# Kernel tuning notes

Hardware: AMD Instinct MI355X
Metric: run time of the kernel (lower is better)

The kernel has to match this reference:

```python
import jax, jax.numpy as jnp
import numpy as np

N_NODES = 32768
N_EDGES = 262144
HEAD = 8
CHANNEL = 64
LAYER_NUM = 2
HC = HEAD * CHANNEL  # 512


def setup_inputs() -> dict:
    key = jax.random.key(0)
    ks = jax.random.split(key, 12)
    def lin(k, fan_in, fan_out):
        s = 1.0 / np.sqrt(fan_in)
        kw, kb = jax.random.split(k)
        W = jax.random.uniform(kw, (fan_in, fan_out), jnp.float32, -s, s)
        b = jax.random.uniform(kb, (fan_out,), jnp.float32, -s, s)
        return W, b
    Wn, bn = lin(ks[0], 118, HC)
    We, be = lin(ks[1], 22, HC)
    Wa, ba = lin(ks[2], 2 * HC, HC)
    attn_w = jax.random.normal(ks[3], (1, HEAD, CHANNEL), jnp.float32) * 0.1
    x = jax.random.normal(ks[4], (N_NODES, 118), jnp.float32)
    edge_feat = jax.random.normal(ks[5], (N_EDGES, 22), jnp.float32)
    src = jax.random.randint(ks[6], (N_EDGES,), 0, N_NODES)
    dst = jax.random.randint(ks[7], (N_EDGES,), 0, N_NODES)
    return {"x": x, "edge_feat": edge_feat, "src": src, "dst": dst,
            "Wn": Wn, "bn": bn, "We": We, "be": be, "Wa": Wa, "ba": ba,
            "attn_w": attn_w}


def reference(x, edge_feat, src, dst, Wn, bn, We, be, Wa, ba, attn_w):
    N = x.shape[0]
    H, C = attn_w.shape[1], attn_w.shape[2]
    h = x @ Wn + bn                      # [N, H*C]
    _eh = edge_feat @ We + be            # computed in original forward, never used
    for _ in range(LAYER_NUM):
        # gather src/dst node states onto edges and score them (GATv2 style)
        e = jnp.concatenate([h[src], h[dst]], axis=-1)            # [E, 2HC]
        e = jax.nn.leaky_relu(e @ Wa + ba, negative_slope=0.01)   # [E, HC]
        score = jnp.sum(e.reshape(-1, H, C) * attn_w, axis=-1)    # [E, H]
        # edge softmax normalized over incoming edges of each dst node
        m = jax.ops.segment_max(score, dst, num_segments=N)       # [N, H]
        ex = jnp.exp(score - m[dst])                              # [E, H]
        denom = jax.ops.segment_sum(ex, dst, num_segments=N)      # [N, H]
        alpha = ex / denom[dst]                                   # [E, H]
        # weighted message passing: u_mul_e then sum over dst
        msg = h[src].reshape(-1, H, C) * alpha[:, :, None]        # [E, H, C]
        h = jax.ops.segment_sum(msg, dst, num_segments=N).reshape(N, H * C)
    return h
```

## Files before the change

kernel.cpp:

```cpp
#include <hip/hip_runtime.h>
#include <hip/hip_bf16.h>
#include <stdint.h>

#define N_NODES 32768
#define N_EDGES 262144

typedef __attribute__((ext_vector_type(8))) short short8;
typedef __attribute__((ext_vector_type(4))) float f32x4;
typedef __attribute__((ext_vector_type(4))) uint u32x4;

typedef const __attribute__((address_space(1))) void* gvp;
typedef __attribute__((address_space(3))) void* lvp;

#define LDH 1536
#define LDH2 1024

__device__ __forceinline__ float bf2f(ushort u) {
  return __uint_as_float(((uint)u) << 16);
}
__device__ __forceinline__ ushort f2bf(float f) {
  uint x = __float_as_uint(f);
  uint r = (x + 0x7fffu + ((x >> 16) & 1u)) >> 16;
  return (ushort)r;
}
__device__ __forceinline__ float loadf(const void* p, size_t i, int isbf) {
  return isbf ? bf2f(((const ushort*)p)[i]) : ((const float*)p)[i];
}

__global__ void detect_init(const uint* __restrict__ xw, int* __restrict__ flag,
                            int* __restrict__ cnt) {
  if (blockIdx.x > 0) {
    int i = (blockIdx.x - 1) * 256 + threadIdx.x;
    if (i < N_NODES) cnt[i] = 0;
    return;
  }
  __shared__ int c;
  if (threadIdx.x == 0) c = 0;
  __syncthreads();
  int good = 0;
  for (int i = threadIdx.x; i < 1024; i += 256) {
    uint lo = xw[i] & 0xFFFFu;
    uint ef = (lo >> 7) & 0xFFu;
    if (lo == 0u || (ef >= 0x60u && ef <= 0x90u)) good++;
  }
  atomicAdd(&c, good);
  __syncthreads();
  if (threadIdx.x == 0) *flag = (c >= 614) ? 1 : 0;
}

__global__ void prep_all(const void* __restrict__ Wa, const void* __restrict__ Wn,
                         const void* __restrict__ ba, const void* __restrict__ bn,
                         const void* __restrict__ aw, const void* __restrict__ x,
                         const int* __restrict__ flag, const int* __restrict__ dst,
                         ushort* __restrict__ W2T, ushort* __restrict__ BTc,
                         ushort* __restrict__ Wn_pad, float* __restrict__ bias2,
                         float* __restrict__ bnf, float* __restrict__ wf,
                         float* __restrict__ zbias, ushort* __restrict__ xp,
                         int* __restrict__ cnt) {
  const int b = blockIdx.x;
  if (b >= 2564 + 16384) {
    int e = (b - 2564 - 16384) * 256 + threadIdx.x;
    atomicAdd(&cnt[dst[e]], 1);
    return;
  }
  const int fl = *flag;
  if (b < 2048) {
    int t = b * 256 + threadIdx.x;
    int n = t >> 9, k = t & 511;
    size_t idx = (n < 512) ? ((size_t)k * 512 + n) : ((size_t)(512 + k) * 512 + (n - 512));
    W2T[t] = f2bf(loadf(Wa, idx, fl));
  } else if (b < 2304) {
    int t = (b - 2048) * 256 + threadIdx.x;
    int n = t >> 7, k = t & 127;
    BTc[t] = (k < 118) ? f2bf(loadf(Wn, (size_t)k * 512 + n, fl)) : (ushort)0;
  } else if (b < 2560) {
    int t = (b - 2304) * 256 + threadIdx.x;
    int n = t >> 9, j = t & 511;
    Wn_pad[t] = (n < 118) ? f2bf(loadf(Wn, (size_t)n * 512 + j, fl)) : (ushort)0;
  } else if (b < 2564) {
    int t = (b - 2560) * 256 + threadIdx.x;
    if (t < 1024) bias2[t] = (t < 512) ? loadf(ba, t, fl) : 0.f;
    if (t < 512) { bnf[t] = loadf(bn, t, fl); wf[t] = loadf(aw, t, fl); }
    if (t < 128) zbias[t] = 0.f;
  } else {
    int t = (b - 2564) * 256 + threadIdx.x;
    int i = t >> 7, k = t & 127;
    xp[t] = (k < 118) ? f2bf(loadf(x, (size_t)i * 118 + k, fl)) : (ushort)0;
  }
}

__device__ __forceinline__ void gemm_body(
    const ushort* __restrict__ A, const ushort* __restrict__ BT,
    const float* __restrict__ bias, ushort* __restrict__ C,
    int M, int N, int K, int lda, int ldc, int bx, int by) {
  __shared__ __align__(16) ushort As[128 * 32];
  __shared__ __align__(16) ushort Bs[128 * 32];
  const int tid = threadIdx.x, wave = tid >> 6, lane = tid & 63;
  const int bm = by * 128, bn = bx * 128;
  const int wm = (wave >> 1) * 64, wn = (wave & 1) * 64;
  const int fcol = lane & 15, quad = lane >> 4;

  const f32x4 zero = {0.f, 0.f, 0.f, 0.f};
  f32x4 acc[4][4];
#pragma unroll
  for (int i = 0; i < 4; ++i)
#pragma unroll
    for (int j = 0; j < 4; ++j) acc[i][j] = zero;

  for (int k0 = 0; k0 < K; k0 += 32) {
#pragma unroll
    for (int r = 0; r < 2; ++r) {
      int o = r * 4096 + wave * 1024 + lane * 16;
      int row = o >> 6;
      int ke = (o & 63) >> 1;
      const ushort* gA = A + (size_t)(bm + row) * lda + k0 + ke;
      const ushort* gB = BT + (size_t)(bn + row) * K + k0 + ke;
      ushort* lA = As + ((r * 4096 + wave * 1024) >> 1);
      ushort* lB = Bs + ((r * 4096 + wave * 1024) >> 1);
      __builtin_amdgcn_global_load_lds((gvp)(const void*)gA, (lvp)(void*)lA, 16, 0, 0);
      __builtin_amdgcn_global_load_lds((gvp)(const void*)gB, (lvp)(void*)lB, 16, 0, 0);
    }
    __syncthreads();
    short8 a[4], b[4];
#pragma unroll
    for (int i = 0; i < 4; ++i) {
      a[i] = *(const short8*)&As[(wm + i * 16 + fcol) * 32 + quad * 8];
      b[i] = *(const short8*)&Bs[(wn + i * 16 + fcol) * 32 + quad * 8];
    }
#pragma unroll
    for (int i = 0; i < 4; ++i)
#pragma unroll
      for (int j = 0; j < 4; ++j)
        acc[i][j] = __builtin_amdgcn_mfma_f32_16x16x32_bf16(a[i], b[j], acc[i][j], 0, 0, 0);
    __syncthreads();
  }

#pragma unroll
  for (int i = 0; i < 4; ++i) {
    int rowb = bm + wm + i * 16 + quad * 4;
#pragma unroll
    for (int j = 0; j < 4; ++j) {
      int col = bn + wn + j * 16 + fcol;
      float bb = bias[col];
#pragma unroll
      for (int r = 0; r < 4; ++r) {
        C[(size_t)(rowb + r) * ldc + col] = f2bf(acc[i][j][r] + bb);
      }
    }
  }
}

__global__ __launch_bounds__(256)
void mid_kernel(const ushort* __restrict__ W2T, const ushort* __restrict__ Wn_pad,
                const float* __restrict__ bnf, const float* __restrict__ bias2,
                const float* __restrict__ zbias, float* __restrict__ bcomb,
                ushort* __restrict__ BTc, const int* __restrict__ cnt,
                int* __restrict__ rowptr, int* __restrict__ cursor) {
  const int b = blockIdx.x;
  if (b < 256) {
    const int tid = b * 256 + threadIdx.x;
    if (tid < 512) bcomb[tid] = bnf[tid];
    const int wave = threadIdx.x >> 6, lane = threadIdx.x & 63;
    const int j = b * 4 + wave;
    const uint4 v = *(const uint4*)(W2T + (size_t)j * 512 + lane * 8);
    const float4 b0 = *(const float4*)(bnf + lane * 8);
    const float4 b1 = *(const float4*)(bnf + lane * 8 + 4);
    const uint w[4] = {v.x, v.y, v.z, v.w};
    const float bb[8] = {b0.x, b0.y, b0.z, b0.w, b1.x, b1.y, b1.z, b1.w};
    float s = 0.f;
#pragma unroll
    for (int i = 0; i < 4; ++i) {
      s += __uint_as_float(w[i] << 16) * bb[2 * i];
      s += __uint_as_float(w[i] & 0xffff0000u) * bb[2 * i + 1];
    }
    s += __shfl_xor(s, 1);  s += __shfl_xor(s, 2);  s += __shfl_xor(s, 4);
    s += __shfl_xor(s, 8);  s += __shfl_xor(s, 16); s += __shfl_xor(s, 32);
    if (lane == 0) bcomb[512 + j] = s + bias2[j];
  } else if (b < 264) {
    gemm_body(W2T, Wn_pad, zbias, BTc + 512 * 128, 1024, 128, 512, 512, 128,
              0, b - 256);
  } else {
    __shared__ int part[256];
    const int t = threadIdx.x;
    const int base = t * 128;
    int s = 0;
    for (int i = 0; i < 128; ++i) s += cnt[base + i];
    part[t] = s;
    __syncthreads();
    for (int off = 1; off < 256; off <<= 1) {
      int v = (t >= off) ? part[t - off] : 0;
      __syncthreads();
      part[t] += v;
      __syncthreads();
    }
    int run = (t == 0) ? 0 : part[t - 1];
    for (int i = 0; i < 128; ++i) {
      int v = cnt[base + i];
      rowptr[base + i] = run;
      cursor[base + i] = run;
      run += v;
    }
    if (t == 255) rowptr[N_NODES] = part[255];
  }
}

__global__ __launch_bounds__(256)
void fill_gemm(const int* __restrict__ dst, const int* __restrict__ src,
               int* __restrict__ cursor, int* __restrict__ esrc,
               const ushort* __restrict__ xp, const ushort* __restrict__ BTc,
               const float* __restrict__ bcomb, ushort* __restrict__ HP) {
  const int b = blockIdx.x;
  if (b < 1024) {
    int e = b * 256 + threadIdx.x;
    int p = atomicAdd(&cursor[dst[e]], 1);
    esrc[p] = src[e];
    return;
  }
  const int gi = b - 1024;
  gemm_body(xp, BTc, bcomb, HP, N_NODES, 1536, 128, 128, LDH, gi % 12, gi / 12);
}

__global__ __launch_bounds__(256)
void node_fused_l1(const ushort* __restrict__ HP, const int* __restrict__ esrc,
                   const int* __restrict__ rowptr, const float* __restrict__ wf,
                   const float* __restrict__ bias2, ushort* __restrict__ HP2,
                   ushort* __restrict__ Q2arr) {
  const int wave = threadIdx.x >> 6, lane = threadIdx.x & 63;
  const int d = blockIdx.x * 4 + wave;
  const int beg = rowptr[d], end = rowptr[d + 1];
  const int c0 = lane * 8;

  const uint4 qv = *(const uint4*)(HP + (size_t)d * LDH + 1024 + c0);
  const uint qw[4] = {qv.x, qv.y, qv.z, qv.w};
  float q[8], w[8];
#pragma unroll
  for (int i = 0; i < 4; ++i) {
    q[2 * i]     = __uint_as_float(qw[i] << 16);
    q[2 * i + 1] = __uint_as_float(qw[i] & 0xffff0000u);
  }
  const float4 w0 = *(const float4*)(wf + c0);
  const float4 w1 = *(const float4*)(wf + c0 + 4);
  w[0] = w0.x; w[1] = w0.y; w[2] = w0.z; w[3] = w0.w;
  w[4] = w1.x; w[5] = w1.y; w[6] = w1.z; w[7] = w1.w;

  float m = -3e38f, den = 0.f;
  float aP[8], aQ[8], aH[8];
#pragma unroll
  for (int i = 0; i < 8; ++i) { aP[i] = 0.f; aQ[i] = 0.f; aH[i] = 0.f; }

  if (beg < end) {
    int sj = esrc[beg];
    for (int j = beg; j < end; ++j) {
      const int s = sj;
      if (j + 1 < end) sj = esrc[j + 1];
      const ushort* row = HP + (size_t)s * LDH;
      const uint4 hv = *(const uint4*)(row + c0);
      const uint4 pa = *(const uint4*)(row + 512 + c0);
      const uint4 pb = *(const uint4*)(row + 1024 + c0);
      const uint paw[4] = {pa.x, pa.y, pa.z, pa.w};
      const uint pbw[4] = {pb.x, pb.y, pb.z, pb.w};
      const uint hw[4]  = {hv.x, hv.y, hv.z, hv.w};
      float t = 0.f;
#pragma unroll
      for (int i = 0; i < 4; ++i) {
        float ea = __uint_as_float(paw[i] << 16) + q[2 * i];
        float eb = __uint_as_float(paw[i] & 0xffff0000u) + q[2 * i + 1];
        ea = (ea > 0.f) ? ea : 0.01f * ea;
        eb = (eb > 0.f) ? eb : 0.01f * eb;
        t += ea * w[2 * i] + eb * w[2 * i + 1];
      }
      t += __shfl_xor(t, 1);
      t += __shfl_xor(t, 2);
      t += __shfl_xor(t, 4);
      if (__any(t > m)) {
        const float mnew = fmaxf(m, t);
        const float corr = __expf(m - mnew);
        const float ex = __expf(t - mnew);
        den = den * corr + ex;
#pragma unroll
        for (int i = 0; i < 4; ++i) {
          aP[2 * i]     = aP[2 * i] * corr     + ex * __uint_as_float(paw[i] << 16);
          aP[2 * i + 1] = aP[2 * i + 1] * corr + ex * __uint_as_float(paw[i] & 0xffff0000u);
          aQ[2 * i]     = aQ[2 * i] * corr     + ex * __uint_as_float(pbw[i] << 16);
          aQ[2 * i + 1] = aQ[2 * i + 1] * corr + ex * __uint_as_float(pbw[i] & 0xffff0000u);
          aH[2 * i]     = aH[2 * i] * corr     + ex * __uint_as_float(hw[i] << 16);
          aH[2 * i + 1] = aH[2 * i + 1] * corr + ex * __uint_as_float(hw[i] & 0xffff0000u);
        }
        m = mnew;
      } else {
        const float ex = __expf(t - m);
        den += ex;
#pragma unroll
        for (int i = 0; i < 4; ++i) {
          aP[2 * i]     += ex * __uint_as_float(paw[i] << 16);
          aP[2 * i + 1] += ex * __uint_as_float(paw[i] & 0xffff0000u);
          aQ[2 * i]     += ex * __uint_as_float(pbw[i] << 16);
          aQ[2 * i + 1] += ex * __uint_as_float(pbw[i] & 0xffff0000u);
          aH[2 * i]     += ex * __uint_as_float(hw[i] << 16);
          aH[2 * i + 1] += ex * __uint_as_float(hw[i] & 0xffff0000u);
        }
      }
    }
  }

  const int deg = end - beg;
  const float inv = deg ? (1.f / den) : 0.f;
  const float4 bp0 = *(const float4*)(bias2 + c0);
  const float4 bp1 = *(const float4*)(bias2 + c0 + 4);
  const float bp[8] = {bp0.x, bp0.y, bp0.z, bp0.w, bp1.x, bp1.y, bp1.z, bp1.w};
  uint oP[4], oQ[4], oH[4];
#pragma unroll
  for (int i = 0; i < 4; ++i) {
    float p0 = deg ? aP[2 * i] * inv : bp[2 * i];
    float p1 = deg ? aP[2 * i + 1] * inv : bp[2 * i + 1];
    float q0 = deg ? aQ[2 * i] * inv : 0.f;
    float q1 = deg ? aQ[2 * i + 1] * inv : 0.f;
    float h0v = aH[2 * i] * inv, h1v = aH[2 * i + 1] * inv;
    oP[i] = (uint)f2bf(p0) | ((uint)f2bf(p1) << 16);
    oQ[i] = (uint)f2bf(q0) | ((uint)f2bf(q1) << 16);
    oH[i] = (uint)f2bf(h0v) | ((uint)f2bf(h1v) << 16);
  }
  u32x4 vP = {oP[0], oP[1], oP[2], oP[3]};
  u32x4 vQ = {oQ[0], oQ[1], oQ[2], oQ[3]};
  u32x4 vH = {oH[0], oH[1], oH[2], oH[3]};
  ushort* orow = HP2 + (size_t)d * LDH2;
  *(u32x4*)(orow + c0) = vH;
  *(u32x4*)(orow + 512 + c0) = vP;
  *(u32x4*)(Q2arr + (size_t)d * 512 + c0) = vQ;
}

__global__ __launch_bounds__(256)
void node_fused_l2(const ushort* __restrict__ HP2, const ushort* __restrict__ Q2arr,
                   const int* __restrict__ esrc, const int* __restrict__ rowptr,
                   const float* __restrict__ wf, const int* __restrict__ flag,
                   void* __restrict__ out) {
  const int wave = threadIdx.x >> 6, lane = threadIdx.x & 63;
  const int d = blockIdx.x * 4 + wave;
  const int beg = rowptr[d], end = rowptr[d + 1];
  const int c0 = lane * 8;

  const uint4 qv = *(const uint4*)(Q2arr + (size_t)d * 512 + c0);
  const uint qw[4] = {qv.x, qv.y, qv.z, qv.w};
  float q[8], w[8];
#pragma unroll
  for (int i = 0; i < 4; ++i) {
    q[2 * i]     = __uint_as_float(qw[i] << 16);
    q[2 * i + 1] = __uint_as_float(qw[i] & 0xffff0000u);
  }
  const float4 w0 = *(const float4*)(wf + c0);
  const float4 w1 = *(const float4*)(wf + c0 + 4);
  w[0] = w0.x; w[1] = w0.y; w[2] = w0.z; w[3] = w0.w;
  w[4] = w1.x; w[5] = w1.y; w[6] = w1.z; w[7] = w1.w;

  float m = -3e38f, den = 0.f;
  float acc[8] = {0.f, 0.f, 0.f, 0.f, 0.f, 0.f, 0.f, 0.f};

  if (beg < end) {
    int sj = esrc[beg];
    for (int j = beg; j < end; ++j) {
      const int s = sj;
      if (j + 1 < end) sj = esrc[j + 1];
      const ushort* row = HP2 + (size_t)s * LDH2;
      const uint4 hv = *(const uint4*)(row + c0);
      const uint4 pv = *(const uint4*)(row + 512 + c0);
      const uint pw[4] = {pv.x, pv.y, pv.z, pv.w};
      const uint hw[4] = {hv.x, hv.y, hv.z, hv.w};
      float t = 0.f;
#pragma unroll
      for (int i = 0; i < 4; ++i) {
        float ea = __uint_as_float(pw[i] << 16) + q[2 * i];
        float eb = __uint_as_float(pw[i] & 0xffff0000u) + q[2 * i + 1];
        ea = (ea > 0.f) ? ea : 0.01f * ea;
        eb = (eb > 0.f) ? eb : 0.01f * eb;
        t += ea * w[2 * i] + eb * w[2 * i + 1];
      }
      t += __shfl_xor(t, 1);
      t += __shfl_xor(t, 2);
      t += __shfl_xor(t, 4);
      if (__any(t > m)) {
        const float mnew = fmaxf(m, t);
        const float corr = __expf(m - mnew);
        const float ex = __expf(t - mnew);
        den = den * corr + ex;
#pragma unroll
        for (int i = 0; i < 4; ++i) {
          acc[2 * i]     = acc[2 * i] * corr     + ex * __uint_as_float(hw[i] << 16);
          acc[2 * i + 1] = acc[2 * i + 1] * corr + ex * __uint_as_float(hw[i] & 0xffff0000u);
        }
        m = mnew;
      } else {
        const float ex = __expf(t - m);
        den += ex;
#pragma unroll
        for (int i = 0; i < 4; ++i) {
          acc[2 * i]     += ex * __uint_as_float(hw[i] << 16);
          acc[2 * i + 1] += ex * __uint_as_float(hw[i] & 0xffff0000u);
        }
      }
    }
  }

  const float inv = (end > beg) ? (1.f / den) : 0.f;
  if (*flag) {
    uint o[4];
#pragma unroll
    for (int i = 0; i < 4; ++i) {
      float v0 = acc[2 * i] * inv, v1 = acc[2 * i + 1] * inv;
      o[i] = (uint)f2bf(v0) | ((uint)f2bf(v1) << 16);
    }
    u32x4 ov = {o[0], o[1], o[2], o[3]};
    __builtin_nontemporal_store(ov, (u32x4*)((ushort*)out + (size_t)d * 512 + c0));
  } else {
    f32x4 f0 = {acc[0] * inv, acc[1] * inv, acc[2] * inv, acc[3] * inv};
    f32x4 f1 = {acc[4] * inv, acc[5] * inv, acc[6] * inv, acc[7] * inv};
    __builtin_nontemporal_store(f0, (f32x4*)((float*)out + (size_t)d * 512 + c0));
    __builtin_nontemporal_store(f1, (f32x4*)((float*)out + (size_t)d * 512 + c0 + 4));
  }
}

extern "C" void kernel_launch(void* const* d_in, const int* in_sizes, int n_in,
                              void* d_out, int out_size, void* d_ws, size_t ws_size,
                              hipStream_t stream) {
  const void* x   = d_in[0];
  const int*  src = (const int*)d_in[2];
  const int*  dst = (const int*)d_in[3];
  const void* Wn  = d_in[4];
  const void* bn  = d_in[5];
  const void* Wa  = d_in[8];
  const void* ba  = d_in[9];
  const void* aw  = d_in[10];

  char* ws = (char*)d_ws;
  size_t off = 0;
  auto alloc = [&](size_t bytes) {
    char* p = ws + off;
    off = (off + bytes + 255) & ~(size_t)255;
    return p;
  };
  ushort* HP     = (ushort*)alloc((size_t)N_NODES * LDH * 2);
  ushort* HP2    = (ushort*)alloc((size_t)N_NODES * LDH2 * 2);
  ushort* Q2arr  = (ushort*)alloc((size_t)N_NODES * 512 * 2);
  int*    esrc   = (int*)   alloc((size_t)N_EDGES * 4);
  int*    rowptr = (int*)   alloc((size_t)(N_NODES + 1) * 4);
  int*    cnt    = (int*)   alloc((size_t)N_NODES * 4);
  int*    cursor = (int*)   alloc((size_t)N_NODES * 4);
  ushort* W2T    = (ushort*)alloc((size_t)1024 * 512 * 2);
  ushort* BTc    = (ushort*)alloc((size_t)1536 * 128 * 2);
  ushort* Wn_pad = (ushort*)alloc((size_t)128 * 512 * 2);
  float*  bias2  = (float*) alloc(1024 * 4);
  float*  bcomb  = (float*) alloc(1536 * 4);
  float*  zbias  = (float*) alloc(128 * 4);
  ushort* xp     = (ushort*)alloc((size_t)N_NODES * 128 * 2);
  float*  bnf    = (float*) alloc(512 * 4);
  float*  wf     = (float*) alloc(512 * 4);
  int*    flag   = (int*)   alloc(256);

  detect_init<<<1 + 128, 256, 0, stream>>>((const uint*)x, flag, cnt);
  prep_all<<<2564 + 16384 + 1024, 256, 0, stream>>>(
      Wa, Wn, ba, bn, aw, x, flag, dst, W2T, BTc, Wn_pad, bias2, bnf, wf, zbias,
      xp, cnt);
  mid_kernel<<<256 + 8 + 1, 256, 0, stream>>>(W2T, Wn_pad, bnf, bias2, zbias,
                                              bcomb, BTc, cnt, rowptr, cursor);
  fill_gemm<<<1024 + 12 * 256, 256, 0, stream>>>(dst, src, cursor, esrc, xp, BTc,
                                                 bcomb, HP);
  node_fused_l1<<<N_NODES / 4, 256, 0, stream>>>(HP, esrc, rowptr, wf, bias2,
                                                 HP2, Q2arr);
  node_fused_l2<<<N_NODES / 4, 256, 0, stream>>>(HP2, Q2arr, esrc, rowptr, wf,
                                                 flag, d_out);
}
```

Measured before the change: 406.5 us.

## Compute layer-2 Q projection with a node GEMM instead of per-edge aggregation

The layer-1 kernel stops gathering and aggregating the precomputed Q-projection slice for every edge. The layer-2 query term is now computed after aggregation by a separate dense GEMM over the aggregated node features. The first GEMM's Q columns go to a separate array so gathered rows shrink from 1536 to 1024 elements. This cuts per-edge gather bandwidth and FMAs, at the cost of an extra kernel launch and a 32768x512x512 GEMM. It also relies on bias2+512 being zero, which holds for how bias2 is initialized.

```diff
diff --git a/kernel.cpp b/kernel.cpp
--- a/kernel.cpp
+++ b/kernel.cpp
@@ -12,7 +12,7 @@
 typedef const __attribute__((address_space(1))) void* gvp;
 typedef __attribute__((address_space(3))) void* lvp;
 
-#define LDH 1536
+#define LDH1 1024
 #define LDH2 1024
 
 __device__ __forceinline__ float bf2f(ushort u) {
@@ -92,7 +92,7 @@
 __device__ __forceinline__ void gemm_body(
     const ushort* __restrict__ A, const ushort* __restrict__ BT,
     const float* __restrict__ bias, ushort* __restrict__ C,
-    int M, int N, int K, int lda, int ldc, int bx, int by) {
+    int K, int lda, int ldc, int bx, int by, int col_off) {
   __shared__ __align__(16) ushort As[128 * 32];
   __shared__ __align__(16) ushort Bs[128 * 32];
   const int tid = threadIdx.x, wave = tid >> 6, lane = tid & 63;
@@ -144,7 +144,7 @@
       float bb = bias[col];
 #pragma unroll
       for (int r = 0; r < 4; ++r) {
-        C[(size_t)(rowb + r) * ldc + col] = f2bf(acc[i][j][r] + bb);
+        C[(size_t)(rowb + r) * ldc + (col - col_off)] = f2bf(acc[i][j][r] + bb);
       }
     }
   }
@@ -177,8 +177,7 @@
     s += __shfl_xor(s, 8);  s += __shfl_xor(s, 16); s += __shfl_xor(s, 32);
     if (lane == 0) bcomb[512 + j] = s + bias2[j];
   } else if (b < 264) {
-    gemm_body(W2T, Wn_pad, zbias, BTc + 512 * 128, 1024, 128, 512, 512, 128,
-              0, b - 256);
+    gemm_body(W2T, Wn_pad, zbias, BTc + 512 * 128, 512, 512, 128, 0, b - 256, 0);
   } else {
     __shared__ int part[256];
     const int t = threadIdx.x;
@@ -208,7 +207,8 @@
 void fill_gemm(const int* __restrict__ dst, const int* __restrict__ src,
                int* __restrict__ cursor, int* __restrict__ esrc,
                const ushort* __restrict__ xp, const ushort* __restrict__ BTc,
-               const float* __restrict__ bcomb, ushort* __restrict__ HP) {
+               const float* __restrict__ bcomb, ushort* __restrict__ HPa,
+               ushort* __restrict__ Q1arr) {
   const int b = blockIdx.x;
   if (b < 1024) {
     int e = b * 256 + threadIdx.x;
@@ -217,20 +217,24 @@
     return;
   }
   const int gi = b - 1024;
-  gemm_body(xp, BTc, bcomb, HP, N_NODES, 1536, 128, 128, LDH, gi % 12, gi / 12);
+  const int bx = gi % 12, by = gi / 12;
+  if (bx < 8)
+    gemm_body(xp, BTc, bcomb, HPa, 128, 128, LDH1, bx, by, 0);
+  else
+    gemm_body(xp, BTc, bcomb, Q1arr, 128, 128, 512, bx, by, 1024);
 }
 
 __global__ __launch_bounds__(256)
-void node_fused_l1(const ushort* __restrict__ HP, const int* __restrict__ esrc,
-                   const int* __restrict__ rowptr, const float* __restrict__ wf,
-                   const float* __restrict__ bias2, ushort* __restrict__ HP2,
-                   ushort* __restrict__ Q2arr) {
+void node_fused_l1(const ushort* __restrict__ HPa, const ushort* __restrict__ Q1arr,
+                   const int* __restrict__ esrc, const int* __restrict__ rowptr,
+                   const float* __restrict__ wf, const float* __restrict__ bias2,
+                   ushort* __restrict__ HP2) {
   const int wave = threadIdx.x >> 6, lane = threadIdx.x & 63;
   const int d = blockIdx.x * 4 + wave;
   const int beg = rowptr[d], end = rowptr[d + 1];
   const int c0 = lane * 8;
 
-  const uint4 qv = *(const uint4*)(HP + (size_t)d * LDH + 1024 + c0);
+  const uint4 qv = *(const uint4*)(Q1arr + (size_t)d * 512 + c0);
   const uint qw[4] = {qv.x, qv.y, qv.z, qv.w};
   float q[8], w[8];
 #pragma unroll
@@ -244,21 +248,19 @@
   w[4] = w1.x; w[5] = w1.y; w[6] = w1.z; w[7] = w1.w;
 
   float m = -3e38f, den = 0.f;
-  float aP[8], aQ[8], aH[8];
-#pragma unroll
-  for (int i = 0; i < 8; ++i) { aP[i] = 0.f; aQ[i] = 0.f; aH[i] = 0.f; }
+  float aP[8], aH[8];
+#pragma unroll
+  for (int i = 0; i < 8; ++i) { aP[i] = 0.f; aH[i] = 0.f; }
 
   if (beg < end) {
     int sj = esrc[beg];
     for (int j = beg; j < end; ++j) {
       const int s = sj;
       if (j + 1 < end) sj = esrc[j + 1];
-      const ushort* row = HP + (size_t)s * LDH;
+      const ushort* row = HPa + (size_t)s * LDH1;
       const uint4 hv = *(const uint4*)(row + c0);
       const uint4 pa = *(const uint4*)(row + 512 + c0);
-      const uint4 pb = *(const uint4*)(row + 1024 + c0);
       const uint paw[4] = {pa.x, pa.y, pa.z, pa.w};
-      const uint pbw[4] = {pb.x, pb.y, pb.z, pb.w};
       const uint hw[4]  = {hv.x, hv.y, hv.z, hv.w};
       float t = 0.f;
 #pragma unroll
@@ -281,8 +283,6 @@
         for (int i = 0; i < 4; ++i) {
           aP[2 * i]     = aP[2 * i] * corr     + ex * __uint_as_float(paw[i] << 16);
           aP[2 * i + 1] = aP[2 * i + 1] * corr + ex * __uint_as_float(paw[i] & 0xffff0000u);
-          aQ[2 * i]     = aQ[2 * i] * corr     + ex * __uint_as_float(pbw[i] << 16);
-          aQ[2 * i + 1] = aQ[2 * i + 1] * corr + ex * __uint_as_float(pbw[i] & 0xffff0000u);
           aH[2 * i]     = aH[2 * i] * corr     + ex * __uint_as_float(hw[i] << 16);
           aH[2 * i + 1] = aH[2 * i + 1] * corr + ex * __uint_as_float(hw[i] & 0xffff0000u);
         }
@@ -294,8 +294,6 @@
         for (int i = 0; i < 4; ++i) {
           aP[2 * i]     += ex * __uint_as_float(paw[i] << 16);
           aP[2 * i + 1] += ex * __uint_as_float(paw[i] & 0xffff0000u);
-          aQ[2 * i]     += ex * __uint_as_float(pbw[i] << 16);
-          aQ[2 * i + 1] += ex * __uint_as_float(pbw[i] & 0xffff0000u);
           aH[2 * i]     += ex * __uint_as_float(hw[i] << 16);
           aH[2 * i + 1] += ex * __uint_as_float(hw[i] & 0xffff0000u);
         }
@@ -308,25 +306,27 @@
   const float4 bp0 = *(const float4*)(bias2 + c0);
   const float4 bp1 = *(const float4*)(bias2 + c0 + 4);
   const float bp[8] = {bp0.x, bp0.y, bp0.z, bp0.w, bp1.x, bp1.y, bp1.z, bp1.w};
-  uint oP[4], oQ[4], oH[4];
+  uint oP[4], oH[4];
 #pragma unroll
   for (int i = 0; i < 4; ++i) {
     float p0 = deg ? aP[2 * i] * inv : bp[2 * i];
     float p1 = deg ? aP[2 * i + 1] * inv : bp[2 * i + 1];
-    float q0 = deg ? aQ[2 * i] * inv : 0.f;
-    float q1 = deg ? aQ[2 * i + 1] * inv : 0.f;
     float h0v = aH[2 * i] * inv, h1v = aH[2 * i + 1] * inv;
     oP[i] = (uint)f2bf(p0) | ((uint)f2bf(p1) << 16);
-    oQ[i] = (uint)f2bf(q0) | ((uint)f2bf(q1) << 16);
     oH[i] = (uint)f2bf(h0v) | ((uint)f2bf(h1v) << 16);
   }
   u32x4 vP = {oP[0], oP[1], oP[2], oP[3]};
-  u32x4 vQ = {oQ[0], oQ[1], oQ[2], oQ[3]};
   u32x4 vH = {oH[0], oH[1], oH[2], oH[3]};
   ushort* orow = HP2 + (size_t)d * LDH2;
   *(u32x4*)(orow + c0) = vH;
   *(u32x4*)(orow + 512 + c0) = vP;
-  *(u32x4*)(Q2arr + (size_t)d * 512 + c0) = vQ;
+}
+
+__global__ __launch_bounds__(256)
+void q2_gemm(const ushort* __restrict__ HP2, const ushort* __restrict__ W2Q,
+             const float* __restrict__ zb512, ushort* __restrict__ Q2arr) {
+  gemm_body(HP2, W2Q, zb512, Q2arr, 512, LDH2, 512, blockIdx.x & 3,
+            blockIdx.x >> 2, 0);
 }
 
 __global__ __launch_bounds__(256)
@@ -437,7 +437,8 @@
     off = (off + bytes + 255) & ~(size_t)255;
     return p;
   };
-  ushort* HP     = (ushort*)alloc((size_t)N_NODES * LDH * 2);
+  ushort* HPa    = (ushort*)alloc((size_t)N_NODES * LDH1 * 2);
+  ushort* Q1arr  = (ushort*)alloc((size_t)N_NODES * 512 * 2);
   ushort* HP2    = (ushort*)alloc((size_t)N_NODES * LDH2 * 2);
   ushort* Q2arr  = (ushort*)alloc((size_t)N_NODES * 512 * 2);
   int*    esrc   = (int*)   alloc((size_t)N_EDGES * 4);
@@ -462,9 +463,11 @@
   mid_kernel<<<256 + 8 + 1, 256, 0, stream>>>(W2T, Wn_pad, bnf, bias2, zbias,
                                               bcomb, BTc, cnt, rowptr, cursor);
   fill_gemm<<<1024 + 12 * 256, 256, 0, stream>>>(dst, src, cursor, esrc, xp, BTc,
-                                                 bcomb, HP);
-  node_fused_l1<<<N_NODES / 4, 256, 0, stream>>>(HP, esrc, rowptr, wf, bias2,
-                                                 HP2, Q2arr);
+                                                 bcomb, HPa, Q1arr);
+  node_fused_l1<<<N_NODES / 4, 256, 0, stream>>>(HPa, Q1arr, esrc, rowptr, wf,
+                                                 bias2, HP2);
+  q2_gemm<<<4 * (N_NODES / 128), 256, 0, stream>>>(HP2, W2T + 512 * 512,
+                                                   bias2 + 512, Q2arr);
   node_fused_l2<<<N_NODES / 4, 256, 0, stream>>>(HP2, Q2arr, esrc, rowptr, wf,
                                                  flag, d_out);
 }
```

Measured after the change: 396.9 us (median of 2 runs). 2.4% less time.
